# Kernel tuning notes

Measured on AMD Instinct MI355X. Metric: run time of the kernel, lower is better.

## Reference

```python
import jax, jax.numpy as jnp
import numpy as np

NEG_SLOPE = 0.2  # PyG GATConv default


def gat_layer(x, W, att_src, att_dst, bias, src, dst, concat):
    # x: [N, F_in]; W: [F_in, H*C]; att_src/att_dst: [H, C]; bias: [H*C] or [C]
    N = x.shape[0]
    H, C = att_src.shape
    h = (x @ W).reshape(N, H, C)                       # [N, H, C]
    a_s = jnp.einsum('nhc,hc->nh', h, att_src)         # [N, H]
    a_d = jnp.einsum('nhc,hc->nh', h, att_dst)
    e = jax.nn.leaky_relu(a_s[src] + a_d[dst], NEG_SLOPE)  # [E, H]
    # segment softmax over incoming edges of each destination node
    m = jax.ops.segment_max(e, dst, num_segments=N)
    m = jnp.where(jnp.isfinite(m), m, 0.0)
    ee = jnp.exp(e - m[dst])
    s = jax.ops.segment_sum(ee, dst, num_segments=N)
    alpha = ee / (s[dst] + 1e-16)                      # [E, H]
    out = jax.ops.segment_sum(h[src] * alpha[:, :, None], dst, num_segments=N)  # [N, H, C]
    out = out.reshape(N, H * C) if concat else out.mean(axis=1)
    return out + bias


def setup_inputs() -> dict:
    key = jax.random.key(0)
    ks = jax.random.split(key, 16)
    N, E, F_IN, NC = 100000, 3200000, 256, 40
    H, C = 8, 8  # hidden GATConv: heads=8, out=8 -> width 64
    inp = {}
    inp['features'] = jax.random.normal(ks[0], (N, F_IN), dtype=jnp.float32)
    inp['edge_index'] = jax.random.randint(ks[1], (2, E), 0, N, dtype=jnp.int64)
    def p(k, shape):
        return jax.random.normal(k, shape, dtype=jnp.float32) * 0.1
    # layer 0: in 256 -> 8 heads x 8 (concat -> 64)
    inp['W0'] = p(ks[2], (F_IN, H * C)); inp['as0'] = p(ks[3], (H, C)); inp['ad0'] = p(ks[4], (H, C)); inp['b0'] = jnp.zeros((H * C,), jnp.float32)
    # layer 1: 64 -> 8 heads x 8 (concat -> 64)
    inp['W1'] = p(ks[5], (H * C, H * C)); inp['as1'] = p(ks[6], (H, C)); inp['ad1'] = p(ks[7], (H, C)); inp['b1'] = jnp.zeros((H * C,), jnp.float32)
    # layer 2: 64 -> 1 head x n_classes (mean/no-concat)
    inp['W2'] = p(ks[8], (H * C, NC)); inp['as2'] = p(ks[9], (1, NC)); inp['ad2'] = p(ks[10], (1, NC)); inp['b2'] = jnp.zeros((NC,), jnp.float32)
    return inp


def reference(features, edge_index, W0, as0, ad0, b0, W1, as1, ad1, b1, W2, as2, ad2, b2):
    N = features.shape[0]
    loops = jnp.arange(N, dtype=edge_index.dtype)  # PyG GATConv adds self-loops by default
    src = jnp.concatenate([edge_index[0], loops])
    dst = jnp.concatenate([edge_index[1], loops])
    x = gat_layer(features, W0, as0, ad0, b0, src, dst, True)
    x = gat_layer(x, W1, as1, ad1, b1, src, dst, True)
    x = gat_layer(x, W2, as2, ad2, b2, src, dst, False)
    return jax.nn.log_softmax(x, axis=-1)
```

## Files before the change

kernel.cpp:

```cpp
#include <hip/hip_runtime.h>
#include <hip/hip_bf16.h>

#define NEG_SLOPE 0.2f
#define LOG2E 1.44269504f
#define EPB 8192
#define MAXBUCK 800

typedef __attribute__((ext_vector_type(8))) short short8;
typedef __attribute__((ext_vector_type(4))) float f32x4;

__device__ __forceinline__ unsigned short f2bf(float x) {
    unsigned u = __float_as_uint(x);
    unsigned r = (u + 0x7FFFu + ((u >> 16) & 1u)) >> 16;
    return (unsigned short)r;
}

__device__ __forceinline__ float fexp2(float x) {
    return __builtin_amdgcn_exp2f(x);
}

__device__ __forceinline__ float readlane_f(float v, int l) {
    return __int_as_float(__builtin_amdgcn_readlane(__float_as_int(v), l));
}


__global__ __launch_bounds__(512) void bucket_hist_k(
    const int* __restrict__ dsts, int* __restrict__ bcnt,
    int* __restrict__ bhist, int E, int nbuck) {
    __shared__ int lh[MAXBUCK];
    int t = threadIdx.x;
    for (int i = t; i < nbuck; i += 512) lh[i] = 0;
    __syncthreads();
    int base = blockIdx.x * EPB;
    int cnt = E - base;
    if (cnt > EPB) cnt = EPB;
    int nq = cnt >> 2;
    const int4* d4p = (const int4*)(dsts + base);
    for (int i = t; i < nq; i += 512) {
        int4 d = d4p[i];
        atomicAdd(&lh[d.x >> 7], 1);
        atomicAdd(&lh[d.y >> 7], 1);
        atomicAdd(&lh[d.z >> 7], 1);
        atomicAdd(&lh[d.w >> 7], 1);
    }
    for (int i = (nq << 2) + t; i < cnt; i += 512)
        atomicAdd(&lh[dsts[base + i] >> 7], 1);
    __syncthreads();
    int* bh = bhist + (size_t)blockIdx.x * MAXBUCK;
    for (int i = t; i < nbuck; i += 512) {
        int c = lh[i];
        bh[i] = c;
        if (c) atomicAdd(&bcnt[i], c);
    }
}

__global__ __launch_bounds__(512) void bucket_scan_k(
    const int* __restrict__ bcnt, int* __restrict__ bptrE,
    int* __restrict__ bcurE, int nbuck) {
    __shared__ int csum[512];
    int t = threadIdx.x;
    int i0 = t * 4;
    int v0 = 0, v1 = 0, v2 = 0, v3 = 0;
    if (i0 < nbuck) v0 = bcnt[i0];
    if (i0 + 1 < nbuck) v1 = bcnt[i0 + 1];
    if (i0 + 2 < nbuck) v2 = bcnt[i0 + 2];
    if (i0 + 3 < nbuck) v3 = bcnt[i0 + 3];
    int s = v0 + v1 + v2 + v3;
    csum[t] = s;
    __syncthreads();
    for (int off = 1; off < 512; off <<= 1) {
        int x = (t >= off) ? csum[t - off] : 0;
        __syncthreads();
        csum[t] += x;
        __syncthreads();
    }
    int base = csum[t] - s;
    if (i0 < nbuck)     { bptrE[i0] = base;     bcurE[i0] = base; }     base += v0;
    if (i0 + 1 < nbuck) { bptrE[i0 + 1] = base; bcurE[i0 + 1] = base; } base += v1;
    if (i0 + 2 < nbuck) { bptrE[i0 + 2] = base; bcurE[i0 + 2] = base; } base += v2;
    if (i0 + 3 < nbuck) { bptrE[i0 + 3] = base; bcurE[i0 + 3] = base; }
}

__global__ __launch_bounds__(512) void bscatter_k(
    const int* __restrict__ srcs, const int* __restrict__ dsts,
    const int* __restrict__ bhist, int* __restrict__ bcurE,
    int* __restrict__ pairs, int E, int nbuck) {
    __shared__ int lh[MAXBUCK];
    __shared__ int lbase[MAXBUCK];
    int t = threadIdx.x;
    const int* bh = bhist + (size_t)blockIdx.x * MAXBUCK;
    for (int i = t; i < nbuck; i += 512) {
        int c = bh[i];
        lbase[i] = c ? atomicAdd(&bcurE[i], c) : 0;
        lh[i] = 0;
    }
    __syncthreads();
    int base = blockIdx.x * EPB;
    int cnt = E - base;
    if (cnt > EPB) cnt = EPB;
    int nq = cnt >> 2;
    const int4* d4p = (const int4*)(dsts + base);
    const int4* s4p = (const int4*)(srcs + base);
    for (int i = t; i < nq; i += 512) {
        int4 d = d4p[i];
        int4 s = s4p[i];
        int b0 = d.x >> 7, b1 = d.y >> 7, b2 = d.z >> 7, b3 = d.w >> 7;
        int r0 = atomicAdd(&lh[b0], 1);
        int r1 = atomicAdd(&lh[b1], 1);
        int r2 = atomicAdd(&lh[b2], 1);
        int r3 = atomicAdd(&lh[b3], 1);
        pairs[lbase[b0] + r0] = (s.x << 7) | (d.x & 127);
        pairs[lbase[b1] + r1] = (s.y << 7) | (d.y & 127);
        pairs[lbase[b2] + r2] = (s.z << 7) | (d.z & 127);
        pairs[lbase[b3] + r3] = (s.w << 7) | (d.w & 127);
    }
    for (int i = (nq << 2) + t; i < cnt; i += 512) {
        int s = srcs[base + i], d = dsts[base + i];
        int r = atomicAdd(&lh[d >> 7], 1);
        pairs[lbase[d >> 7] + r] = (s << 7) | (d & 127);
    }
}

__global__ __launch_bounds__(256) void bucket_sort_k(
    const int* __restrict__ pairs, const int* __restrict__ bptrE,
    const int* __restrict__ bcurE, int* __restrict__ row_ptr,
    int* __restrict__ csr_src, int N, int Etot) {
    __shared__ int lh[128];
    __shared__ int sc[128];
    int b = blockIdx.x;
    int n0 = b << 7;
    int t = threadIdx.x;
    if (t < 128) lh[t] = 0;
    __syncthreads();
    int e0 = bptrE[b], e1 = bcurE[b];
    for (int e = e0 + t; e < e1; e += 256)
        atomicAdd(&lh[pairs[e] & 127], 1);
    __syncthreads();
    if (t < 128) sc[t] = lh[t];
    __syncthreads();
    for (int off = 1; off < 128; off <<= 1) {
        int x = (t < 128 && t >= off) ? sc[t - off] : 0;
        __syncthreads();
        if (t < 128) sc[t] += x;
        __syncthreads();
    }
    if (t < 128) {
        int cntv = lh[t];
        int excl = sc[t] - cntv;
        int n = n0 + t;
        int rp = e0 + n0 + t + excl;
        if (n < N) {
            row_ptr[n] = rp;
            csr_src[rp] = n << 7;
        }
        lh[t] = rp + 1;
    }
    __syncthreads();
    for (int e = e0 + t; e < e1; e += 256) {
        int p = pairs[e];
        int pos = atomicAdd(&lh[p & 127], 1);
        csr_src[pos] = p & ~127;
    }
    if (b == 0 && t == 0) row_ptr[N] = Etot;
}


template <int K>
__global__ __launch_bounds__(256) void gemm_pack8_k(
    const float* __restrict__ x, const float* __restrict__ W,
    const float* __restrict__ a_src, const float* __restrict__ a_dst,
    char* __restrict__ hrec, float* __restrict__ asb,
    float* __restrict__ adb, int N) {
    constexpr int NT = 4;
    constexpr int KT = K / 32;
    constexpr size_t WF_BYTES = (size_t)KT * NT * 64 * 8 * sizeof(short);
    constexpr size_t H_BYTES = (size_t)64 * 65 * sizeof(float);
    __shared__ alignas(16) char smem[WF_BYTES > H_BYTES ? WF_BYTES : H_BYTES];
    short* Wf = (short*)smem;
    float* hL = (float*)smem;
    int tid = threadIdx.x;
    for (int f = tid; f < KT * NT * 64; f += 256) {
        int lane = f & 63;
        int ntk = f >> 6;
        int nt = ntk % NT, kt = ntk / NT;
        int q = lane >> 4, c = lane & 15;
        int n = nt * 16 + c;
        int k0 = kt * 32 + q * 8;
        short8 frag;
        #pragma unroll
        for (int j = 0; j < 8; ++j)
            frag[j] = (short)f2bf(W[(size_t)(k0 + j) * 64 + n]);
        *(short8*)&Wf[f * 8] = frag;
    }
    __syncthreads();
    int wave = tid >> 6, lane = tid & 63;
    int q = lane >> 4, c = lane & 15;
    int m0 = blockIdx.x * 64 + wave * 16;
    int arow = m0 + c;
    int arl = arow < N ? arow : N - 1;
    f32x4 acc[NT] = {};
    for (int kt = 0; kt < KT; ++kt) {
        const float* xp = x + (size_t)arl * K + kt * 32 + q * 8;
        float4 a0 = *(const float4*)xp;
        float4 a1 = *(const float4*)(xp + 4);
        float av[8] = {a0.x, a0.y, a0.z, a0.w, a1.x, a1.y, a1.z, a1.w};
        short8 af;
        #pragma unroll
        for (int j = 0; j < 8; ++j) af[j] = (short)f2bf(av[j]);
        #pragma unroll
        for (int nt = 0; nt < NT; ++nt) {
            short8 bf = *(const short8*)&Wf[((kt * NT + nt) * 64 + lane) * 8];
            acc[nt] = __builtin_amdgcn_mfma_f32_16x16x32_bf16(af, bf, acc[nt],
                                                              0, 0, 0);
        }
    }
    __syncthreads();
    int lrow = wave * 16 + q * 4;
    #pragma unroll
    for (int nt = 0; nt < NT; ++nt)
        #pragma unroll
        for (int reg = 0; reg < 4; ++reg)
            hL[(lrow + reg) * 65 + nt * 16 + c] = acc[nt][reg];
    __syncthreads();
    #pragma unroll
    for (int it = 0; it < 2; ++it) {
        int id = it * 256 + tid;
        int ln = id >> 3, hd = id & 7;
        int gn = blockIdx.x * 64 + ln;
        if (gn >= N) continue;
        const float* hp = &hL[ln * 65 + hd * 8];
        float as = 0.f, ad = 0.f;
        float hv[8];
        #pragma unroll
        for (int j = 0; j < 8; ++j) {
            hv[j] = hp[j];
            as += hv[j] * a_src[hd * 8 + j];
            ad += hv[j] * a_dst[hd * 8 + j];
        }
        adb[gn * 8 + hd] = ad * LOG2E;
        asb[gn * 8 + hd] = as * LOG2E;
        unsigned short u[8];
        #pragma unroll
        for (int j = 0; j < 8; ++j) u[j] = f2bf(hv[j]);
        uint4 pk;
        pk.x = (unsigned)u[0] | ((unsigned)u[1] << 16);
        pk.y = (unsigned)u[2] | ((unsigned)u[3] << 16);
        pk.z = (unsigned)u[4] | ((unsigned)u[5] << 16);
        pk.w = (unsigned)u[6] | ((unsigned)u[7] << 16);
        *(uint4*)(hrec + (size_t)gn * 128 + hd * 16) = pk;
    }
}


__global__ __launch_bounds__(256) void gemm_pack40_k(
    const float* __restrict__ x, const float* __restrict__ W,
    const float* __restrict__ a_src, const float* __restrict__ a_dst,
    char* __restrict__ rec40, float* __restrict__ adb, int N) {
    constexpr int K = 64, NT = 3, KT = 2;
    constexpr size_t WF_BYTES = (size_t)KT * NT * 64 * 8 * sizeof(short);
    constexpr size_t H_BYTES = (size_t)64 * 41 * sizeof(float);
    __shared__ alignas(16) char smem[WF_BYTES > H_BYTES ? WF_BYTES : H_BYTES];
    short* Wf = (short*)smem;
    float* hL = (float*)smem;
    int tid = threadIdx.x;
    for (int f = tid; f < KT * NT * 64; f += 256) {
        int lane = f & 63;
        int ntk = f >> 6;
        int nt = ntk % NT, kt = ntk / NT;
        int q = lane >> 4, c = lane & 15;
        int n = nt * 16 + c;
        int k0 = kt * 32 + q * 8;
        short8 frag;
        #pragma unroll
        for (int j = 0; j < 8; ++j) {
            float v = (n < 40) ? W[(size_t)(k0 + j) * 40 + n] : 0.f;
            frag[j] = (short)f2bf(v);
        }
        *(short8*)&Wf[f * 8] = frag;
    }
    __syncthreads();
    int wave = tid >> 6, lane = tid & 63;
    int q = lane >> 4, c = lane & 15;
    int m0 = blockIdx.x * 64 + wave * 16;
    int arow = m0 + c;
    int arl = arow < N ? arow : N - 1;
    f32x4 acc[NT] = {};
    for (int kt = 0; kt < KT; ++kt) {
        const float* xp = x + (size_t)arl * K + kt * 32 + q * 8;
        float4 a0 = *(const float4*)xp;
        float4 a1 = *(const float4*)(xp + 4);
        float av[8] = {a0.x, a0.y, a0.z, a0.w, a1.x, a1.y, a1.z, a1.w};
        short8 af;
        #pragma unroll
        for (int j = 0; j < 8; ++j) af[j] = (short)f2bf(av[j]);
        #pragma unroll
        for (int nt = 0; nt < NT; ++nt) {
            short8 bf = *(const short8*)&Wf[((kt * NT + nt) * 64 + lane) * 8];
            acc[nt] = __builtin_amdgcn_mfma_f32_16x16x32_bf16(af, bf, acc[nt],
                                                              0, 0, 0);
        }
    }
    __syncthreads();
    int lrow = wave * 16 + q * 4;
    #pragma unroll
    for (int nt = 0; nt < NT; ++nt) {
        int n = nt * 16 + c;
        if (n >= 40) continue;
        #pragma unroll
        for (int reg = 0; reg < 4; ++reg)
            hL[(lrow + reg) * 41 + n] = acc[nt][reg];
    }
    __syncthreads();
    int ln = tid >> 2, sub = tid & 3;
    int gn = blockIdx.x * 64 + ln;
    float pas = 0.f, pad = 0.f;
    if (gn < N) {
        for (int j = sub; j < 40; j += 4) {
            float hv = hL[ln * 41 + j];
            pas += hv * a_src[j];
            pad += hv * a_dst[j];
        }
    }
    pas += __shfl_xor(pas, 1); pas += __shfl_xor(pas, 2);
    pad += __shfl_xor(pad, 1); pad += __shfl_xor(pad, 2);
    if (gn < N && sub == 0) {
        *(float*)(rec40 + (size_t)gn * 128 + 80) = pas * LOG2E;
        adb[gn] = pad * LOG2E;
    }
    for (int i = tid; i < 64 * 40; i += 256) {
        int n2 = i / 40, ch = i % 40;
        int g2 = blockIdx.x * 64 + n2;
        if (g2 < N)
            *(unsigned short*)(rec40 + (size_t)g2 * 128 + ch * 2) =
                f2bf(hL[n2 * 41 + ch]);
    }
}


#define EDGE64(SUF, IDX)                                                     \
    int s##SUF = __builtin_amdgcn_readlane(sv, (IDX));                       \
    float w##SUF = lwp[(IDX)];                                               \
    unsigned u##SUF =                                                        \
        *(const unsigned short*)(hrec + (size_t)(unsigned)s##SUF + lane2);

__global__ __launch_bounds__(256) void aggr64_k(
    const char* __restrict__ hrec, const float* __restrict__ asb,
    const float* __restrict__ adb, const int* __restrict__ row_ptr,
    const int* __restrict__ csr_src, const float* __restrict__ bias,
    float* __restrict__ out, int N) {
    __shared__ float wlds[4 * 1040];
    int wave = threadIdx.x >> 6;
    int node = blockIdx.x * 4 + wave;
    if (node >= N) return;
    int lane = threadIdx.x & 63;
    int hd = lane >> 3;
    int lane2 = lane * 2;
    float* wbA = wlds + wave * 1040;
    float* wbB = wbA + 520;
    const float* lwpA = wbA + hd * 65;
    const float* lwpB = wbB + hd * 65;
    int beg = row_ptr[node], end = row_ptr[node + 1];
    float4 adv0 = *(const float4*)(adb + (size_t)node * 8);
    float4 adv1 = *(const float4*)(adb + (size_t)node * 8 + 4);
    float acc0 = 0.f, acc1 = 0.f, acc2 = 0.f, acc3 = 0.f;
    float acc4 = 0.f, acc5 = 0.f, acc6 = 0.f, acc7 = 0.f;
    float l0 = 0.f, l1 = 0.f, l2 = 0.f, l3 = 0.f;
    float l4 = 0.f, l5 = 0.f, l6 = 0.f, l7 = 0.f;
    int par = 0;
    for (int i0 = beg; i0 < end; i0 += 64, par ^= 1) {
        int tail = end - i0;
        int sv = csr_src[i0 + (lane < tail ? lane : 0)];
        int cnt = tail < 64 ? tail : 64;
        float* wb = par ? wbB : wbA;
        const float* lwp = par ? lwpB : lwpA;
        {
            const float* asp =
                (const float*)((const char*)asb + (((unsigned)sv) >> 2));
            float4 s0 = *(const float4*)asp;
            float4 s1 = *(const float4*)(asp + 4);
            float w0 = s0.x + adv0.x; w0 = fmaxf(w0, NEG_SLOPE * w0); w0 = fexp2(w0);
            float w1 = s0.y + adv0.y; w1 = fmaxf(w1, NEG_SLOPE * w1); w1 = fexp2(w1);
            float w2 = s0.z + adv0.z; w2 = fmaxf(w2, NEG_SLOPE * w2); w2 = fexp2(w2);
            float w3 = s0.w + adv0.w; w3 = fmaxf(w3, NEG_SLOPE * w3); w3 = fexp2(w3);
            float w4 = s1.x + adv1.x; w4 = fmaxf(w4, NEG_SLOPE * w4); w4 = fexp2(w4);
            float w5 = s1.y + adv1.y; w5 = fmaxf(w5, NEG_SLOPE * w5); w5 = fexp2(w5);
            float w6 = s1.z + adv1.z; w6 = fmaxf(w6, NEG_SLOPE * w6); w6 = fexp2(w6);
            float w7 = s1.w + adv1.w; w7 = fmaxf(w7, NEG_SLOPE * w7); w7 = fexp2(w7);
            if (lane >= cnt) {
                w0 = 0.f; w1 = 0.f; w2 = 0.f; w3 = 0.f;
                w4 = 0.f; w5 = 0.f; w6 = 0.f; w7 = 0.f;
            }
            wb[lane]       = w0;
            wb[65 + lane]  = w1;
            wb[130 + lane] = w2;
            wb[195 + lane] = w3;
            wb[260 + lane] = w4;
            wb[325 + lane] = w5;
            wb[390 + lane] = w6;
            wb[455 + lane] = w7;
        }
        for (int j = 0; j < cnt; j += 8) {
            EDGE64(A, j)      EDGE64(B, j + 1) EDGE64(C, j + 2) EDGE64(D, j + 3)
            EDGE64(E2, j + 4) EDGE64(F, j + 5) EDGE64(G, j + 6) EDGE64(H2, j + 7)
            l0 += wA; l1 += wB; l2 += wC; l3 += wD;
            l4 += wE2; l5 += wF; l6 += wG; l7 += wH2;
            acc0 = fmaf(wA, __uint_as_float(uA << 16), acc0);
            acc1 = fmaf(wB, __uint_as_float(uB << 16), acc1);
            acc2 = fmaf(wC, __uint_as_float(uC << 16), acc2);
            acc3 = fmaf(wD, __uint_as_float(uD << 16), acc3);
            acc4 = fmaf(wE2, __uint_as_float(uE2 << 16), acc4);
            acc5 = fmaf(wF, __uint_as_float(uF << 16), acc5);
            acc6 = fmaf(wG, __uint_as_float(uG << 16), acc6);
            acc7 = fmaf(wH2, __uint_as_float(uH2 << 16), acc7);
        }
    }
    float l = ((l0 + l1) + (l2 + l3)) + ((l4 + l5) + (l6 + l7));
    float acc = ((acc0 + acc1) + (acc2 + acc3)) + ((acc4 + acc5) + (acc6 + acc7));
    out[(size_t)node * 64 + lane] = acc / (l + 1e-16f) + bias[lane];
}


#define F40(SUF, IDX)                                                        \
    int s##SUF = __builtin_amdgcn_readlane(sv, (IDX));                       \
    float w##SUF = readlane_f(wv, (IDX));                                    \
    unsigned u##SUF =                                                        \
        *(const unsigned short*)(rec40 + (size_t)(unsigned)s##SUF + cl2);

__global__ __launch_bounds__(256) void aggr40_k(
    const char* __restrict__ rec40, const float* __restrict__ adb,
    const int* __restrict__ row_ptr, const int* __restrict__ csr_src,
    const float* __restrict__ bias, float* __restrict__ out, int N) {
    int node = blockIdx.x * 4 + (threadIdx.x >> 6);
    if (node >= N) return;
    int lane = threadIdx.x & 63;
    int cl2 = (lane < 40 ? lane : 0) * 2;
    int beg = row_ptr[node], end = row_ptr[node + 1];
    float ad = adb[node];
    float acc0 = 0.f, acc1 = 0.f, acc2 = 0.f, acc3 = 0.f;
    float acc4 = 0.f, acc5 = 0.f, acc6 = 0.f, acc7 = 0.f;
    float lpart = 0.f;
    for (int i0 = beg; i0 < end; i0 += 64) {
        int tail = end - i0;
        int sv = csr_src[i0 + (lane < tail ? lane : 0)];
        int cnt = tail < 64 ? tail : 64;
        float as = *(const float*)(rec40 + (size_t)(unsigned)sv + 80);
        float v = as + ad;
        v = fmaxf(v, NEG_SLOPE * v);
        float wv = fexp2(v);
        wv = (lane < cnt) ? wv : 0.f;
        lpart += wv;
        for (int j = 0; j < cnt; j += 8) {
            F40(A, j)     F40(B, j + 1) F40(C, j + 2) F40(D, j + 3)
            F40(E2, j + 4) F40(F, j + 5) F40(G, j + 6) F40(H2, j + 7)
            acc0 = fmaf(wA, __uint_as_float(uA << 16), acc0);
            acc1 = fmaf(wB, __uint_as_float(uB << 16), acc1);
            acc2 = fmaf(wC, __uint_as_float(uC << 16), acc2);
            acc3 = fmaf(wD, __uint_as_float(uD << 16), acc3);
            acc4 = fmaf(wE2, __uint_as_float(uE2 << 16), acc4);
            acc5 = fmaf(wF, __uint_as_float(uF << 16), acc5);
            acc6 = fmaf(wG, __uint_as_float(uG << 16), acc6);
            acc7 = fmaf(wH2, __uint_as_float(uH2 << 16), acc7);
        }
    }
    #pragma unroll
    for (int off = 32; off > 0; off >>= 1) lpart += __shfl_xor(lpart, off);
    float l = lpart;
    float acc = ((acc0 + acc1) + (acc2 + acc3)) + ((acc4 + acc5) + (acc6 + acc7));
    float val = acc / (l + 1e-16f) + ((lane < 40) ? bias[lane] : 0.f);
    float mval = (lane < 40) ? val : -1e30f;
    #pragma unroll
    for (int off = 32; off > 0; off >>= 1)
        mval = fmaxf(mval, __shfl_xor(mval, off));
    float ex = (lane < 40) ? __expf(val - mval) : 0.f;
    #pragma unroll
    for (int off = 32; off > 0; off >>= 1) ex += __shfl_xor(ex, off);
    if (lane < 40)
        out[(size_t)node * 40 + lane] = val - mval - __logf(ex);
}


extern "C" void kernel_launch(void* const* d_in, const int* in_sizes, int n_in,
                              void* d_out, int out_size, void* d_ws,
                              size_t ws_size, hipStream_t stream) {
    const float* features = (const float*)d_in[0];
    const int* edge_index = (const int*)d_in[1];
    const float* W0 = (const float*)d_in[2];
    const float* as0 = (const float*)d_in[3];
    const float* ad0 = (const float*)d_in[4];
    const float* b0 = (const float*)d_in[5];
    const float* W1 = (const float*)d_in[6];
    const float* as1 = (const float*)d_in[7];
    const float* ad1 = (const float*)d_in[8];
    const float* b1 = (const float*)d_in[9];
    const float* W2 = (const float*)d_in[10];
    const float* as2 = (const float*)d_in[11];
    const float* ad2 = (const float*)d_in[12];
    const float* b2 = (const float*)d_in[13];

    int N = in_sizes[0] / 256;
    int E = in_sizes[1] / 2;
    int Etot = E + N;
    int nbuck = (N + 127) >> 7;
    const int* srcs = edge_index;
    const int* dsts = edge_index + E;

    float* ws = (float*)d_ws;
    float* Hbuf = ws;
    float* Abuf = Hbuf + (size_t)N * 64;
    float* adb  = Abuf + (size_t)N * 64;
    float* asb  = adb + (size_t)N * 8;
    char* hrec  = (char*)(asb + (size_t)N * 8);
    int* row_ptr = (int*)(hrec + (size_t)N * 128);
    int* bcnt    = row_ptr + (N + 2);
    int* bptrE   = bcnt + MAXBUCK;
    int* bcurE   = bptrE + MAXBUCK;
    int* csr_src = bcurE + MAXBUCK;
    int* bhist   = csr_src + Etot;
    int* pairs   = (int*)Hbuf;

    const int B = 256;
    int gAg = (N + 3) / 4;
    int gGm = (N + 63) / 64;
    int gSc = (E + EPB - 1) / EPB;

    (void)hipMemsetAsync(bcnt, 0, MAXBUCK * 4, stream);
    bucket_hist_k<<<gSc, 512, 0, stream>>>(dsts, bcnt, bhist, E, nbuck);
    bucket_scan_k<<<1, 512, 0, stream>>>(bcnt, bptrE, bcurE, nbuck);
    bscatter_k<<<gSc, 512, 0, stream>>>(srcs, dsts, bhist, bcurE, pairs, E,
                                        nbuck);
    bucket_sort_k<<<nbuck, B, 0, stream>>>(pairs, bptrE, bcurE, row_ptr,
                                           csr_src, N, Etot);

    gemm_pack8_k<256><<<gGm, B, 0, stream>>>(features, W0, as0, ad0, hrec,
                                             asb, adb, N);
    aggr64_k<<<gAg, B, 0, stream>>>(hrec, asb, adb, row_ptr, csr_src, b0,
                                    Abuf, N);

    gemm_pack8_k<64><<<gGm, B, 0, stream>>>(Abuf, W1, as1, ad1, hrec, asb,
                                            adb, N);
    aggr64_k<<<gAg, B, 0, stream>>>(hrec, asb, adb, row_ptr, csr_src, b1,
                                    Abuf, N);

    gemm_pack40_k<<<gGm, B, 0, stream>>>(Abuf, W2, as2, ad2, hrec, adb, N);
    aggr40_k<<<gAg, B, 0, stream>>>(hrec, adb, row_ptr, csr_src, b2,
                                    (float*)d_out, N);
}
```

Before: 575.1 us.

## Gather 16-byte feature chunks per lane across 8 edges in aggregation kernels

Both aggregation kernels switch from one 2-byte bf16 gather per lane per edge to a layout where each group of 8 lanes handles one edge and each lane loads a 16-byte chunk of eight channels. Edge indices are spread with ds_bpermute and the weights are read from LDS. Partial sums are then reduced across lane groups with xor shuffles, and the 40-channel kernel stages its results through LDS. The goal is fewer, wider memory transactions per edge and fewer scalar readlanes. The cost is extra cross-lane reductions, an LDS epilogue, and wasted lanes in the 40-channel case (5 of 8 lanes active per edge).

```diff
diff --git a/kernel.cpp b/kernel.cpp
--- a/kernel.cpp
+++ b/kernel.cpp
@@ -17,10 +17,6 @@
 
 __device__ __forceinline__ float fexp2(float x) {
     return __builtin_amdgcn_exp2f(x);
-}
-
-__device__ __forceinline__ float readlane_f(float v, int l) {
-    return __int_as_float(__builtin_amdgcn_readlane(__float_as_int(v), l));
 }
 
 
@@ -337,42 +333,48 @@
 }
 
 
-#define EDGE64(SUF, IDX)                                                     \
-    int s##SUF = __builtin_amdgcn_readlane(sv, (IDX));                       \
-    float w##SUF = lwp[(IDX)];                                               \
-    unsigned u##SUF =                                                        \
-        *(const unsigned short*)(hrec + (size_t)(unsigned)s##SUF + lane2);
+#define G64(SUF, JB)                                                          \
+    int sv##SUF = __builtin_amdgcn_ds_bpermute((JB) * 4 + g4, sv);            \
+    float w##SUF = wb[(JB) + wofs];                                           \
+    uint4 hv##SUF =                                                           \
+        *(const uint4*)(gbase + (size_t)(unsigned)sv##SUF + hoff);
+
+#define FMA8(SUF, LS)                                                         \
+    LS;                                                                       \
+    acc0 = fmaf(w##SUF, __uint_as_float(hv##SUF.x << 16), acc0);              \
+    acc1 = fmaf(w##SUF, __uint_as_float(hv##SUF.x & 0xFFFF0000u), acc1);      \
+    acc2 = fmaf(w##SUF, __uint_as_float(hv##SUF.y << 16), acc2);              \
+    acc3 = fmaf(w##SUF, __uint_as_float(hv##SUF.y & 0xFFFF0000u), acc3);      \
+    acc4 = fmaf(w##SUF, __uint_as_float(hv##SUF.z << 16), acc4);              \
+    acc5 = fmaf(w##SUF, __uint_as_float(hv##SUF.z & 0xFFFF0000u), acc5);      \
+    acc6 = fmaf(w##SUF, __uint_as_float(hv##SUF.w << 16), acc6);              \
+    acc7 = fmaf(w##SUF, __uint_as_float(hv##SUF.w & 0xFFFF0000u), acc7);
 
 __global__ __launch_bounds__(256) void aggr64_k(
     const char* __restrict__ hrec, const float* __restrict__ asb,
     const float* __restrict__ adb, const int* __restrict__ row_ptr,
     const int* __restrict__ csr_src, const float* __restrict__ bias,
     float* __restrict__ out, int N) {
-    __shared__ float wlds[4 * 1040];
+    __shared__ float wlds[4 * 544];
     int wave = threadIdx.x >> 6;
     int node = blockIdx.x * 4 + wave;
     if (node >= N) return;
     int lane = threadIdx.x & 63;
-    int hd = lane >> 3;
-    int lane2 = lane * 2;
-    float* wbA = wlds + wave * 1040;
-    float* wbB = wbA + 520;
-    const float* lwpA = wbA + hd * 65;
-    const float* lwpB = wbB + hd * 65;
+    const char* gbase = hrec;
+    float* wb = wlds + wave * 544;
+    int g4 = (lane >> 3) * 4;
+    int hoff = (lane & 7) * 16;
+    int wofs = (lane & 7) * 68 + (lane >> 3);
     int beg = row_ptr[node], end = row_ptr[node + 1];
     float4 adv0 = *(const float4*)(adb + (size_t)node * 8);
     float4 adv1 = *(const float4*)(adb + (size_t)node * 8 + 4);
     float acc0 = 0.f, acc1 = 0.f, acc2 = 0.f, acc3 = 0.f;
     float acc4 = 0.f, acc5 = 0.f, acc6 = 0.f, acc7 = 0.f;
-    float l0 = 0.f, l1 = 0.f, l2 = 0.f, l3 = 0.f;
-    float l4 = 0.f, l5 = 0.f, l6 = 0.f, l7 = 0.f;
-    int par = 0;
-    for (int i0 = beg; i0 < end; i0 += 64, par ^= 1) {
+    float lpart = 0.f;
+    for (int i0 = beg; i0 < end; i0 += 64) {
         int tail = end - i0;
         int sv = csr_src[i0 + (lane < tail ? lane : 0)];
         int cnt = tail < 64 ? tail : 64;
-        float* wb = par ? wbB : wbA;
-        const float* lwp = par ? lwpB : lwpA;
         {
             const float* asp =
                 (const float*)((const char*)asb + (((unsigned)sv) >> 2));
@@ -390,50 +392,80 @@
                 w0 = 0.f; w1 = 0.f; w2 = 0.f; w3 = 0.f;
                 w4 = 0.f; w5 = 0.f; w6 = 0.f; w7 = 0.f;
             }
-            wb[lane]       = w0;
-            wb[65 + lane]  = w1;
-            wb[130 + lane] = w2;
-            wb[195 + lane] = w3;
-            wb[260 + lane] = w4;
-            wb[325 + lane] = w5;
-            wb[390 + lane] = w6;
-            wb[455 + lane] = w7;
-        }
-        for (int j = 0; j < cnt; j += 8) {
-            EDGE64(A, j)      EDGE64(B, j + 1) EDGE64(C, j + 2) EDGE64(D, j + 3)
-            EDGE64(E2, j + 4) EDGE64(F, j + 5) EDGE64(G, j + 6) EDGE64(H2, j + 7)
-            l0 += wA; l1 += wB; l2 += wC; l3 += wD;
-            l4 += wE2; l5 += wF; l6 += wG; l7 += wH2;
-            acc0 = fmaf(wA, __uint_as_float(uA << 16), acc0);
-            acc1 = fmaf(wB, __uint_as_float(uB << 16), acc1);
-            acc2 = fmaf(wC, __uint_as_float(uC << 16), acc2);
-            acc3 = fmaf(wD, __uint_as_float(uD << 16), acc3);
-            acc4 = fmaf(wE2, __uint_as_float(uE2 << 16), acc4);
-            acc5 = fmaf(wF, __uint_as_float(uF << 16), acc5);
-            acc6 = fmaf(wG, __uint_as_float(uG << 16), acc6);
-            acc7 = fmaf(wH2, __uint_as_float(uH2 << 16), acc7);
-        }
-    }
-    float l = ((l0 + l1) + (l2 + l3)) + ((l4 + l5) + (l6 + l7));
-    float acc = ((acc0 + acc1) + (acc2 + acc3)) + ((acc4 + acc5) + (acc6 + acc7));
-    out[(size_t)node * 64 + lane] = acc / (l + 1e-16f) + bias[lane];
-}
-
-
-#define F40(SUF, IDX)                                                        \
-    int s##SUF = __builtin_amdgcn_readlane(sv, (IDX));                       \
-    float w##SUF = readlane_f(wv, (IDX));                                    \
-    unsigned u##SUF =                                                        \
-        *(const unsigned short*)(rec40 + (size_t)(unsigned)s##SUF + cl2);
+            wb[lane]          = w0;
+            wb[68 + lane]     = w1;
+            wb[2 * 68 + lane] = w2;
+            wb[3 * 68 + lane] = w3;
+            wb[4 * 68 + lane] = w4;
+            wb[5 * 68 + lane] = w5;
+            wb[6 * 68 + lane] = w6;
+            wb[7 * 68 + lane] = w7;
+        }
+        int j = 0;
+        for (; j + 32 <= cnt; j += 32) {
+            G64(A, j) G64(B, j + 8) G64(C, j + 16) G64(D, j + 24)
+            FMA8(A, lpart += wA) FMA8(B, lpart += wB)
+            FMA8(C, lpart += wC) FMA8(D, lpart += wD)
+        }
+        for (; j < cnt; j += 8) {
+            G64(A, j)
+            FMA8(A, lpart += wA)
+        }
+    }
+    #pragma unroll
+    for (int m = 8; m <= 32; m <<= 1) {
+        acc0 += __shfl_xor(acc0, m);
+        acc1 += __shfl_xor(acc1, m);
+        acc2 += __shfl_xor(acc2, m);
+        acc3 += __shfl_xor(acc3, m);
+        acc4 += __shfl_xor(acc4, m);
+        acc5 += __shfl_xor(acc5, m);
+        acc6 += __shfl_xor(acc6, m);
+        acc7 += __shfl_xor(acc7, m);
+        lpart += __shfl_xor(lpart, m);
+    }
+    if (lane < 8) {
+        float denom = lpart + 1e-16f;
+        const float4 b0 = *(const float4*)(bias + lane * 8);
+        const float4 b1 = *(const float4*)(bias + lane * 8 + 4);
+        float4 o0, o1;
+        o0.x = acc0 / denom + b0.x;
+        o0.y = acc1 / denom + b0.y;
+        o0.z = acc2 / denom + b0.z;
+        o0.w = acc3 / denom + b0.w;
+        o1.x = acc4 / denom + b1.x;
+        o1.y = acc5 / denom + b1.y;
+        o1.z = acc6 / denom + b1.z;
+        o1.w = acc7 / denom + b1.w;
+        float* op = out + (size_t)node * 64 + lane * 8;
+        *(float4*)op = o0;
+        *(float4*)(op + 4) = o1;
+    }
+}
+
+
+#define G40(SUF, JB)                                                          \
+    int sv##SUF = __builtin_amdgcn_ds_bpermute((JB) * 4 + g4, sv);            \
+    float w##SUF = wb[(JB) + gof];                                            \
+    uint4 hv##SUF =                                                           \
+        *(const uint4*)(gbase + (size_t)(unsigned)sv##SUF + hoff);
 
 __global__ __launch_bounds__(256) void aggr40_k(
     const char* __restrict__ rec40, const float* __restrict__ adb,
     const int* __restrict__ row_ptr, const int* __restrict__ csr_src,
     const float* __restrict__ bias, float* __restrict__ out, int N) {
-    int node = blockIdx.x * 4 + (threadIdx.x >> 6);
+    __shared__ float wlds[4 * 104];
+    int wave = threadIdx.x >> 6;
+    int node = blockIdx.x * 4 + wave;
     if (node >= N) return;
     int lane = threadIdx.x & 63;
-    int cl2 = (lane < 40 ? lane : 0) * 2;
+    const char* gbase = rec40;
+    float* wb = wlds + wave * 104;
+    float* epi = wb + 64;
+    int g4 = (lane >> 3) * 4;
+    int sub = lane & 7;
+    int hoff = (sub < 5 ? sub : 0) * 16;
+    int gof = lane >> 3;
     int beg = row_ptr[node], end = row_ptr[node + 1];
     float ad = adb[node];
     float acc0 = 0.f, acc1 = 0.f, acc2 = 0.f, acc3 = 0.f;
@@ -449,24 +481,37 @@
         float wv = fexp2(v);
         wv = (lane < cnt) ? wv : 0.f;
         lpart += wv;
-        for (int j = 0; j < cnt; j += 8) {
-            F40(A, j)     F40(B, j + 1) F40(C, j + 2) F40(D, j + 3)
-            F40(E2, j + 4) F40(F, j + 5) F40(G, j + 6) F40(H2, j + 7)
-            acc0 = fmaf(wA, __uint_as_float(uA << 16), acc0);
-            acc1 = fmaf(wB, __uint_as_float(uB << 16), acc1);
-            acc2 = fmaf(wC, __uint_as_float(uC << 16), acc2);
-            acc3 = fmaf(wD, __uint_as_float(uD << 16), acc3);
-            acc4 = fmaf(wE2, __uint_as_float(uE2 << 16), acc4);
-            acc5 = fmaf(wF, __uint_as_float(uF << 16), acc5);
-            acc6 = fmaf(wG, __uint_as_float(uG << 16), acc6);
-            acc7 = fmaf(wH2, __uint_as_float(uH2 << 16), acc7);
-        }
+        wb[lane] = wv;
+        int j = 0;
+        for (; j + 32 <= cnt; j += 32) {
+            G40(A, j) G40(B, j + 8) G40(C, j + 16) G40(D, j + 24)
+            FMA8(A, ) FMA8(B, ) FMA8(C, ) FMA8(D, )
+        }
+        for (; j < cnt; j += 8) {
+            G40(A, j)
+            FMA8(A, )
+        }
+    }
+    #pragma unroll
+    for (int m = 8; m <= 32; m <<= 1) {
+        acc0 += __shfl_xor(acc0, m);
+        acc1 += __shfl_xor(acc1, m);
+        acc2 += __shfl_xor(acc2, m);
+        acc3 += __shfl_xor(acc3, m);
+        acc4 += __shfl_xor(acc4, m);
+        acc5 += __shfl_xor(acc5, m);
+        acc6 += __shfl_xor(acc6, m);
+        acc7 += __shfl_xor(acc7, m);
     }
     #pragma unroll
     for (int off = 32; off > 0; off >>= 1) lpart += __shfl_xor(lpart, off);
     float l = lpart;
-    float acc = ((acc0 + acc1) + (acc2 + acc3)) + ((acc4 + acc5) + (acc6 + acc7));
-    float val = acc / (l + 1e-16f) + ((lane < 40) ? bias[lane] : 0.f);
+    if (lane < 5) {
+        *(float4*)&epi[lane * 8] = make_float4(acc0, acc1, acc2, acc3);
+        *(float4*)&epi[lane * 8 + 4] = make_float4(acc4, acc5, acc6, acc7);
+    }
+    float accv = (lane < 40) ? epi[lane] : 0.f;
+    float val = accv / (l + 1e-16f) + ((lane < 40) ? bias[lane] : 0.f);
     float mval = (lane < 40) ? val : -1e30f;
     #pragma unroll
     for (int off = 32; off > 0; off >>= 1)
```

New measurement: 552.1 us. 1.04x faster.
